# Kernel optimization log

Hardware: AMD Instinct MI355X
Metric: run time of the kernel (lower is better)

The kernel has to match this reference:

```python
import jax, jax.numpy as jnp
import numpy as np

QUERY_DIM = 1024
KEY_DIM = 1024
NUM_HEADS = 16
HEAD_DIM = QUERY_DIM // NUM_HEADS


def setup_inputs() -> dict:
    key = jax.random.key(0)
    ks = jax.random.split(key, 11)
    B, Sq, Sk = 2, 2048, 2048
    s = 0.02
    return {
        "q": jax.random.normal(ks[0], (B, Sq, QUERY_DIM), jnp.float32),
        "k": jax.random.normal(ks[1], (B, Sk, KEY_DIM), jnp.float32),
        "v": jax.random.normal(ks[2], (B, Sk, KEY_DIM), jnp.float32),
        "Wq": jax.random.normal(ks[3], (QUERY_DIM, QUERY_DIM), jnp.float32) * s,
        "bq": jnp.zeros((QUERY_DIM,), jnp.float32),
        "Wk": jax.random.normal(ks[4], (KEY_DIM, QUERY_DIM), jnp.float32) * s,
        "bk": jnp.zeros((QUERY_DIM,), jnp.float32),
        "Wv": jax.random.normal(ks[5], (KEY_DIM, QUERY_DIM), jnp.float32) * s,
        "bv": jnp.zeros((QUERY_DIM,), jnp.float32),
        "Wo": jax.random.normal(ks[6], (QUERY_DIM, QUERY_DIM), jnp.float32) * s,
        "bo": jnp.zeros((QUERY_DIM,), jnp.float32),
    }


def reference(q, k, v, Wq, bq, Wk, bk, Wv, bv, Wo, bo):
    B, Sq, _ = q.shape
    Sk = k.shape[1]
    scale = HEAD_DIM ** -0.5
    # projections -> [B, H, S, Dh]
    qh = (q @ Wq + bq).reshape(B, Sq, NUM_HEADS, HEAD_DIM).transpose(0, 2, 1, 3)
    kh = (k @ Wk + bk).reshape(B, Sk, NUM_HEADS, HEAD_DIM).transpose(0, 2, 1, 3)
    vh = (v @ Wv + bv).reshape(B, Sk, NUM_HEADS, HEAD_DIM).transpose(0, 2, 1, 3)
    scores = jnp.einsum("bhqd,bhkd->bhqk", qh, kh) * scale
    attn = jax.nn.softmax(scores, axis=-1)
    out = jnp.einsum("bhqk,bhkd->bhqd", attn, vh)
    out = out.transpose(0, 2, 1, 3).reshape(B, Sq, QUERY_DIM)
    return out @ Wo + bo  # dropout is identity at inference
```

## Files before the change

### kernel.cpp

```cpp
#include <hip/hip_runtime.h>
#include <hip/hip_fp16.h>
#include <cstddef>


#define B_   2
#define S_   2048
#define D_   1024
#define H_   16
#define DH_  64

typedef _Float16 half8 __attribute__((ext_vector_type(8)));
typedef _Float16 half4 __attribute__((ext_vector_type(4)));
typedef _Float16 half2v __attribute__((ext_vector_type(2)));
typedef float floatx4 __attribute__((ext_vector_type(4)));
typedef float floatx16 __attribute__((ext_vector_type(16)));
typedef int intx4 __attribute__((ext_vector_type(4)));

#define MFMA32(a, b, c) __builtin_amdgcn_mfma_f32_16x16x32_f16((a), (b), (c), 0, 0, 0)
#define MFMA3216(a, b, c) __builtin_amdgcn_mfma_f32_32x32x16_f16((a), (b), (c), 0, 0, 0)

#if __has_builtin(__builtin_amdgcn_fdot2)
#define LP_FDOT2 1
#else
#define LP_FDOT2 0
#endif

__device__ __forceinline__ void half_swap(int& a, int& b, const int hi) {
#if __has_builtin(__builtin_amdgcn_permlane32_swap)
    (void)hi;
    auto r = __builtin_amdgcn_permlane32_swap(a, b, false, false);
    a = r[0]; b = r[1];
#else
    const int ax = __shfl_xor(a, 32, 64), bx = __shfl_xor(b, 32, 64);
    const int na = hi ? bx : a;
    b = hi ? b : ax;
    a = na;
#endif
}

__global__ __launch_bounds__(256) void prep(
    const float* __restrict__ q, const float* __restrict__ k,
    const float* __restrict__ v,
    __half* __restrict__ qf, __half* __restrict__ kf, __half* __restrict__ vf,
    const float* __restrict__ Wq, const float* __restrict__ Wk,
    const float* __restrict__ Wv, const float* __restrict__ Wo,
    __half* __restrict__ Wtq, __half* __restrict__ Wtk,
    __half* __restrict__ Wtv, __half* __restrict__ Wto)
{
    __shared__ __align__(16) __half T[64][72];
    const int tid = threadIdx.x;
    const int z = blockIdx.z;
    if (z < 3) {
        const float* srcs[3] = {q, k, v};
        __half* dsts[3] = {qf, kf, vf};
        const int i = blockIdx.x * 256 + tid;
        const float4* s = (const float4*)srcs[z];
        const float4 a = s[2 * i], b = s[2 * i + 1];
        half8 h;
        h[0] = (_Float16)a.x; h[1] = (_Float16)a.y; h[2] = (_Float16)a.z; h[3] = (_Float16)a.w;
        h[4] = (_Float16)b.x; h[5] = (_Float16)b.y; h[6] = (_Float16)b.z; h[7] = (_Float16)b.w;
        *(half8*)&dsts[z][(size_t)i * 8] = h;
        return;
    }
    if (blockIdx.x >= 256) return;
    const float* Ws[4] = {Wq, Wk, Wv, Wo};
    __half* Wts[4] = {Wtq, Wtk, Wtv, Wto};
    const int n0 = (blockIdx.x & 15) * 64, k0 = (blockIdx.x >> 4) * 64;
    for (int w = 0; w < 4; ++w) {
        const float* W = Ws[w];
        __half* Wt = Wts[w];
        #pragma unroll
        for (int p = 0; p < 4; ++p) {
            const int c = tid + p * 256;
            const int kr = c >> 4, nc = (c & 15) * 4;
            const float4 a = *(const float4*)&W[(size_t)(k0 + kr) * D_ + n0 + nc];
            T[nc + 0][kr] = __float2half(a.x);
            T[nc + 1][kr] = __float2half(a.y);
            T[nc + 2][kr] = __float2half(a.z);
            T[nc + 3][kr] = __float2half(a.w);
        }
        __syncthreads();
        #pragma unroll
        for (int p = 0; p < 2; ++p) {
            const int c = tid + p * 256;
            const int nr = c >> 3, kc = (c & 7) * 8;
            *(half8*)&Wt[(size_t)(n0 + nr) * D_ + k0 + kc] = *(const half8*)&T[nr][kc];
        }
        __syncthreads();
    }
}

__device__ __forceinline__ void gemm_core(
    const __half* __restrict__ A, const __half* __restrict__ Bt,
    const float* __restrict__ bias, void* __restrict__ dst,
    const int mode, const float oscale)
{
    __shared__ __align__(16) char gsm[36864];
    __half (*As)[72] = (__half(*)[72])gsm;
    __half (*Bs)[72] = (__half(*)[72])(gsm + 18432);

    const int tid = threadIdx.x;
    const int m0 = blockIdx.y * 128, n0 = blockIdx.x * 128;
    const int lane = tid & 63, wv = tid >> 6;
    const int quad = lane >> 4, lr = lane & 15;
    const int wm0 = (wv >> 1) * 64, wn0 = (wv & 1) * 64;

    floatx4 acc[4][4];
    #pragma unroll
    for (int i = 0; i < 4; ++i)
        #pragma unroll
        for (int j = 0; j < 4; ++j)
            acc[i][j] = (floatx4){0.f, 0.f, 0.f, 0.f};

    half8 pa[4], pb[4];
    #pragma unroll
    for (int p = 0; p < 4; ++p) {
        const int c = tid + p * 256;
        const int row = c >> 3, seg = (c & 7) * 8;
        pa[p] = *(const half8*)&A [(size_t)(m0 + row) * D_ + seg];
        pb[p] = *(const half8*)&Bt[(size_t)(n0 + row) * D_ + seg];
    }

    for (int k0 = 0; k0 < D_; k0 += 64) {
        __syncthreads();
        #pragma unroll
        for (int p = 0; p < 4; ++p) {
            const int c = tid + p * 256;
            const int row = c >> 3, seg = (c & 7) * 8;
            *(half8*)&As[row][seg] = pa[p];
            *(half8*)&Bs[row][seg] = pb[p];
        }
        if (k0 + 64 < D_) {
            #pragma unroll
            for (int p = 0; p < 4; ++p) {
                const int c = tid + p * 256;
                const int row = c >> 3, seg = (c & 7) * 8;
                pa[p] = *(const half8*)&A [(size_t)(m0 + row) * D_ + k0 + 64 + seg];
                pb[p] = *(const half8*)&Bt[(size_t)(n0 + row) * D_ + k0 + 64 + seg];
            }
        }
        __syncthreads();
        #pragma unroll
        for (int ks = 0; ks < 2; ++ks) {
            const int ko = quad * 8 + ks * 32;
            half8 af[4], bf[4];
            #pragma unroll
            for (int i = 0; i < 4; ++i) af[i] = *(const half8*)&As[wm0 + i * 16 + lr][ko];
            #pragma unroll
            for (int j = 0; j < 4; ++j) bf[j] = *(const half8*)&Bs[wn0 + j * 16 + lr][ko];
            #pragma unroll
            for (int i = 0; i < 4; ++i)
                #pragma unroll
                for (int j = 0; j < 4; ++j)
                    acc[i][j] = MFMA32(af[i], bf[j], acc[i][j]);
        }
    }

    if (mode == 1) {
        float* out = (float*)dst;
        #pragma unroll
        for (int i = 0; i < 4; ++i) {
            #pragma unroll
            for (int j = 0; j < 4; ++j) {
                const int col = n0 + wn0 + j * 16 + lr;
                const float bval = bias[col];
                #pragma unroll
                for (int r = 0; r < 4; ++r) {
                    const int m = m0 + wm0 + i * 16 + quad * 4 + r;
                    out[(size_t)m * D_ + col] = acc[i][j][r] + bval;
                }
            }
        }
        return;
    }

    __syncthreads();
    __half (*Ct)[136] = (__half(*)[136])gsm;
    #pragma unroll
    for (int i = 0; i < 4; ++i) {
        #pragma unroll
        for (int j = 0; j < 4; ++j) {
            const int nl = wn0 + j * 16 + lr;
            const float bval = bias[n0 + nl];
            #pragma unroll
            for (int r = 0; r < 4; ++r) {
                const int ml = wm0 + i * 16 + quad * 4 + r;
                const _Float16 hv = (_Float16)((acc[i][j][r] + bval) * oscale);
                if (mode == 0) Ct[ml][nl] = hv;
                else           Ct[nl][ml] = hv;
            }
        }
    }
    __syncthreads();
    __half* oh = (__half*)dst;
    #pragma unroll
    for (int p = 0; p < 8; ++p) {
        const int row = (tid >> 4) + p * 16;
        const int cs  = (tid & 15) * 8;
        const half8 vls = *(const half8*)&Ct[row][cs];
        if (mode == 0) {
            const int m = m0 + row, col = n0 + cs;
            const int b = m >> 11, s = m & (S_ - 1);
            const int h = col >> 6, d = col & 63;
            *(half8*)&oh[(((size_t)(b * H_ + h) * S_ + s) << 6) + d] = vls;
        } else {
            const int col = n0 + row, m = m0 + cs;
            const int b = m >> 11, s = m & (S_ - 1);
            const int h = col >> 6, d = col & 63;
            *(half8*)&oh[((size_t)(b * H_ + h) * DH_ + d) * S_ + s] = vls;
        }
    }
}

__global__ __launch_bounds__(256) void gemm_proj(
    const __half* __restrict__ qf, const __half* __restrict__ kf,
    const __half* __restrict__ vf,
    const __half* __restrict__ Wtq, const __half* __restrict__ Wtk,
    const __half* __restrict__ Wtv,
    const float* __restrict__ bq, const float* __restrict__ bk,
    const float* __restrict__ bv,
    __half* __restrict__ qhf, __half* __restrict__ khf, __half* __restrict__ vht)
{
    const __half* As[3] = {qf, kf, vf};
    const __half* Bts[3] = {Wtq, Wtk, Wtv};
    const float* bs[3] = {bq, bk, bv};
    __half* ds[3] = {qhf, khf, vht};
    const int z = blockIdx.z;
    gemm_core(As[z], Bts[z], bs[z], ds[z], z == 2 ? 2 : 0,
              z == 0 ? 0.1803368801111244f : 1.0f);
}

__global__ __launch_bounds__(256) void gemm_final(
    const __half* __restrict__ attf, const __half* __restrict__ Wto,
    const float* __restrict__ bo, float* __restrict__ out)
{
    gemm_core(attf, Wto, bo, out, 1, 1.0f);
}

__global__ __launch_bounds__(512, 4) void attn_f16(
    const __half* __restrict__ qhf, const __half* __restrict__ khf,
    const __half* __restrict__ vht, __half* __restrict__ attf)
{
    __shared__ __align__(16) char smem[36864];

    const int tid = threadIdx.x;
    const int lane = tid & 63, wv = tid >> 6;
    const int l31 = lane & 31, hi = lane >> 5;
    const int kb = wv >> 2, qb = wv & 3;
    const int bh = blockIdx.y;
    const int q0 = blockIdx.x * 128;
    const size_t hbase = (size_t)bh * S_ * DH_;

    half8 qB[4];
    #pragma unroll
    for (int ds = 0; ds < 4; ++ds)
        qB[ds] = *(const half8*)&qhf[hbase
            + (size_t)(q0 + qb * 32 + l31) * DH_ + ds * 16 + hi * 8];

    float lp0 = 0.f, lp1 = 0.f;
#if !LP_FDOT2
    float lp2 = 0.f, lp3 = 0.f;
#endif
    floatx16 O[2];
    #pragma unroll
    for (int i = 0; i < 16; ++i) { O[0][i] = 0.f; O[1][i] = 0.f; }

    const int srow = tid >> 3, sseg = (tid & 7) * 8;
    const __half* kg = khf + hbase + (size_t)srow * DH_ + sseg;
    const __half* vg = vht + hbase + (size_t)srow * S_ + sseg;

    {
        __half (*K0)[72] = (__half(*)[72])smem;
        __half (*V0)[72] = (__half(*)[72])(smem + 9216);
        *(half8*)&K0[srow][sseg] = *(const half8*)kg;
        *(half8*)&V0[srow][sseg] = *(const half8*)vg;
    }
    kg += 64 * DH_; vg += 64;
    half8 pk = *(const half8*)kg;
    half8 pv = *(const half8*)vg;
    __syncthreads();

    const half2v one2 = {(_Float16)1.0f, (_Float16)1.0f};

    for (int kt = 0; kt < S_; kt += 64) {
        const int cb = (kt >> 6) & 1;
        __half (*Ks)[72] = (__half(*)[72])(smem + cb * 18432);
        __half (*Vs)[72] = (__half(*)[72])(smem + cb * 18432 + 9216);
        __half (*Kn)[72] = (__half(*)[72])(smem + (cb ^ 1) * 18432);
        __half (*Vn)[72] = (__half(*)[72])(smem + (cb ^ 1) * 18432 + 9216);

        if (kt + 64 < S_) {
            *(half8*)&Kn[srow][sseg] = pk;
            *(half8*)&Vn[srow][sseg] = pv;
            if (kt + 128 < S_) {
                kg += 64 * DH_; vg += 64;
                pk = *(const half8*)kg;
                pv = *(const half8*)vg;
            }
        }

        floatx16 s;
        #pragma unroll
        for (int i = 0; i < 16; ++i) s[i] = 0.f;
        __builtin_amdgcn_s_setprio(1);
        #pragma unroll
        for (int ds = 0; ds < 4; ++ds) {
            const half8 aK = *(const half8*)&Ks[kb * 32 + l31][ds * 16 + hi * 8];
            s = MFMA3216(aK, qB[ds], s);
        }
        __builtin_amdgcn_s_setprio(0);

        #pragma unroll
        for (int r = 0; r < 16; ++r) {
            const float e = __builtin_amdgcn_exp2f(s[r]);
#if !LP_FDOT2
            (r & 2) ? ((r & 1) ? (lp3 += e) : (lp2 += e))
                    : ((r & 1) ? (lp1 += e) : (lp0 += e));
#endif
            s[r] = e;
        }

        half8 pB[2];
        int PW[2][4];
        #pragma unroll
        for (int ks = 0; ks < 2; ++ks) {
            int P0 = __builtin_bit_cast(int, __builtin_amdgcn_cvt_pkrtz(s[ks * 8 + 0], s[ks * 8 + 1]));
            int P1 = __builtin_bit_cast(int, __builtin_amdgcn_cvt_pkrtz(s[ks * 8 + 2], s[ks * 8 + 3]));
            int P2 = __builtin_bit_cast(int, __builtin_amdgcn_cvt_pkrtz(s[ks * 8 + 4], s[ks * 8 + 5]));
            int P3 = __builtin_bit_cast(int, __builtin_amdgcn_cvt_pkrtz(s[ks * 8 + 6], s[ks * 8 + 7]));
            half_swap(P0, P2, hi);
            half_swap(P1, P3, hi);
            PW[ks][0] = P0; PW[ks][1] = P1; PW[ks][2] = P2; PW[ks][3] = P3;
            const intx4 w = {P0, P1, P2, P3};
            pB[ks] = __builtin_bit_cast(half8, w);
        }

        __builtin_amdgcn_s_setprio(1);
        #pragma unroll
        for (int db = 0; db < 2; ++db)
            #pragma unroll
            for (int ks = 0; ks < 2; ++ks) {
                const half8 aV = *(const half8*)&Vs[db * 32 + l31][kb * 32 + ks * 16 + hi * 8];
                O[db] = MFMA3216(aV, pB[ks], O[db]);
            }
        __builtin_amdgcn_s_setprio(0);

#if LP_FDOT2
        #pragma unroll
        for (int ks = 0; ks < 2; ++ks) {
            lp0 = __builtin_amdgcn_fdot2(__builtin_bit_cast(half2v, PW[ks][0]), one2, lp0, false);
            lp1 = __builtin_amdgcn_fdot2(__builtin_bit_cast(half2v, PW[ks][1]), one2, lp1, false);
            lp0 = __builtin_amdgcn_fdot2(__builtin_bit_cast(half2v, PW[ks][2]), one2, lp0, false);
            lp1 = __builtin_amdgcn_fdot2(__builtin_bit_cast(half2v, PW[ks][3]), one2, lp1, false);
        }
#endif

        __syncthreads();
    }

    float (*R)[132] = (float(*)[132])smem;
    float* Lred = (float*)(smem + 33792);

#if LP_FDOT2
    float lp = lp0 + lp1;
#else
    float lp = (lp0 + lp1) + (lp2 + lp3);
#endif
    lp += __shfl_xor(lp, 32, 64);
    const int qg = qb * 32 + l31;
    if (lane < 32) Lred[kb * 128 + qg] = lp;
    if (kb == 1) {
        #pragma unroll
        for (int db = 0; db < 2; ++db)
            #pragma unroll
            for (int r = 0; r < 16; ++r) {
                const int d = db * 32 + (r & 3) + 8 * (r >> 2) + 4 * hi;
                R[d][qg] = O[db][r];
            }
    }
    __syncthreads();
    if (kb == 0) {
        const float il = 1.0f / (Lred[qg] + Lred[128 + qg]);
        #pragma unroll
        for (int db = 0; db < 2; ++db)
            #pragma unroll
            for (int r = 0; r < 16; ++r) {
                const int d = db * 32 + (r & 3) + 8 * (r >> 2) + 4 * hi;
                O[db][r] = (O[db][r] + R[d][qg]) * il;
            }
    }
    __syncthreads();
    __half (*F)[72] = (__half(*)[72])smem;
    if (kb == 0) {
        #pragma unroll
        for (int db = 0; db < 2; ++db)
            #pragma unroll
            for (int t = 0; t < 4; ++t) {
                half4 hv;
                #pragma unroll
                for (int r = 0; r < 4; ++r) hv[r] = (_Float16)O[db][t * 4 + r];
                *(half4*)&F[qg][db * 32 + t * 8 + hi * 4] = hv;
            }
    }
    __syncthreads();

    const int b = bh >> 4, h = bh & 15;
    const int qrow = tid >> 2, dseg = (tid & 3) * 16;
    __half* dstp = &attf[(((size_t)(b * S_ + q0 + qrow)) << 10) + h * DH_ + dseg];
    *(half8*)&dstp[0] = *(const half8*)&F[qrow][dseg];
    *(half8*)&dstp[8] = *(const half8*)&F[qrow][dseg + 8];
}

extern "C" void kernel_launch(void* const* d_in, const int* in_sizes, int n_in,
                              void* d_out, int out_size, void* d_ws, size_t ws_size,
                              hipStream_t stream) {
    const float* q  = (const float*)d_in[0];
    const float* k  = (const float*)d_in[1];
    const float* v  = (const float*)d_in[2];
    const float* Wq = (const float*)d_in[3];
    const float* bq = (const float*)d_in[4];
    const float* Wk = (const float*)d_in[5];
    const float* bk = (const float*)d_in[6];
    const float* Wv = (const float*)d_in[7];
    const float* bv = (const float*)d_in[8];
    const float* Wo = (const float*)d_in[9];
    const float* bo = (const float*)d_in[10];
    float* out = (float*)d_out;

    __half* ws = (__half*)d_ws;
    const size_t NE = (size_t)B_ * S_ * D_;
    __half* qf   = ws;
    __half* kf   = ws + NE;
    __half* vf   = ws + 2 * NE;
    __half* qhf  = ws + 3 * NE;
    __half* khf  = ws + 4 * NE;
    __half* vht  = ws + 5 * NE;
    __half* attf = ws + 6 * NE;
    __half* Wtq  = ws + 7 * NE;
    __half* Wtk  = Wtq + (size_t)D_ * D_;
    __half* Wtv  = Wtk + (size_t)D_ * D_;
    __half* Wto  = Wtv + (size_t)D_ * D_;

    const dim3 blk(256);
    prep<<<dim3((unsigned)(NE / 8 / 256), 1, 4), blk, 0, stream>>>(
        q, k, v, qf, kf, vf, Wq, Wk, Wv, Wo, Wtq, Wtk, Wtv, Wto);

    gemm_proj<<<dim3(D_ / 128, (B_ * S_) / 128, 3), blk, 0, stream>>>(
        qf, kf, vf, Wtq, Wtk, Wtv, bq, bk, bv, qhf, khf, vht);

    attn_f16<<<dim3(S_ / 128, B_ * H_), dim3(512), 0, stream>>>(qhf, khf, vht, attf);

    gemm_final<<<dim3(D_ / 128, (B_ * S_) / 128), blk, 0, stream>>>(attf, Wto, bo, out);
}
```

Before: 225.1 us.

## Double-buffer GEMM LDS tiles and remap block indices for XCD locality

New measurement: 222.7 us. Within noise of the previous version (-1.0%).

```diff
diff --git a/kernel.cpp b/kernel.cpp
--- a/kernel.cpp
+++ b/kernel.cpp
@@ -93,14 +93,11 @@
 __device__ __forceinline__ void gemm_core(
     const __half* __restrict__ A, const __half* __restrict__ Bt,
     const float* __restrict__ bias, void* __restrict__ dst,
-    const int mode, const float oscale)
+    const int mode, const float oscale, const int m0, const int n0)
 {
-    __shared__ __align__(16) char gsm[36864];
-    __half (*As)[72] = (__half(*)[72])gsm;
-    __half (*Bs)[72] = (__half(*)[72])(gsm + 18432);
+    extern __shared__ __align__(16) char gsm[];
 
     const int tid = threadIdx.x;
-    const int m0 = blockIdx.y * 128, n0 = blockIdx.x * 128;
     const int lane = tid & 63, wv = tid >> 6;
     const int quad = lane >> 4, lr = lane & 15;
     const int wm0 = (wv >> 1) * 64, wn0 = (wv & 1) * 64;
@@ -111,6 +108,8 @@
         #pragma unroll
         for (int j = 0; j < 4; ++j)
             acc[i][j] = (floatx4){0.f, 0.f, 0.f, 0.f};
+
+    const int srow = tid >> 3, sseg = (tid & 7) * 8;
 
     half8 pa[4], pb[4];
     #pragma unroll
@@ -120,26 +119,53 @@
         pa[p] = *(const half8*)&A [(size_t)(m0 + row) * D_ + seg];
         pb[p] = *(const half8*)&Bt[(size_t)(n0 + row) * D_ + seg];
     }
-
-    for (int k0 = 0; k0 < D_; k0 += 64) {
-        __syncthreads();
+    {
+        __half (*As0)[72] = (__half(*)[72])gsm;
+        __half (*Bs0)[72] = (__half(*)[72])(gsm + 18432);
         #pragma unroll
         for (int p = 0; p < 4; ++p) {
             const int c = tid + p * 256;
             const int row = c >> 3, seg = (c & 7) * 8;
-            *(half8*)&As[row][seg] = pa[p];
-            *(half8*)&Bs[row][seg] = pb[p];
-        }
+            *(half8*)&As0[row][seg] = pa[p];
+            *(half8*)&Bs0[row][seg] = pb[p];
+        }
+    }
+    #pragma unroll
+    for (int p = 0; p < 4; ++p) {
+        const int c = tid + p * 256;
+        const int row = c >> 3, seg = (c & 7) * 8;
+        pa[p] = *(const half8*)&A [(size_t)(m0 + row) * D_ + 64 + seg];
+        pb[p] = *(const half8*)&Bt[(size_t)(n0 + row) * D_ + 64 + seg];
+    }
+    __syncthreads();
+
+    for (int k0 = 0; k0 < D_; k0 += 64) {
+        const int cb = (k0 >> 6) & 1;
+        __half (*As)[72] = (__half(*)[72])(gsm + cb * 36864);
+        __half (*Bs)[72] = (__half(*)[72])(gsm + cb * 36864 + 18432);
+        __half (*An)[72] = (__half(*)[72])(gsm + (cb ^ 1) * 36864);
+        __half (*Bn)[72] = (__half(*)[72])(gsm + (cb ^ 1) * 36864 + 18432);
+
         if (k0 + 64 < D_) {
             #pragma unroll
             for (int p = 0; p < 4; ++p) {
                 const int c = tid + p * 256;
                 const int row = c >> 3, seg = (c & 7) * 8;
-                pa[p] = *(const half8*)&A [(size_t)(m0 + row) * D_ + k0 + 64 + seg];
-                pb[p] = *(const half8*)&Bt[(size_t)(n0 + row) * D_ + k0 + 64 + seg];
-            }
-        }
-        __syncthreads();
+                *(half8*)&An[row][seg] = pa[p];
+                *(half8*)&Bn[row][seg] = pb[p];
+            }
+            if (k0 + 128 < D_) {
+                #pragma unroll
+                for (int p = 0; p < 4; ++p) {
+                    const int c = tid + p * 256;
+                    const int row = c >> 3, seg = (c & 7) * 8;
+                    pa[p] = *(const half8*)&A [(size_t)(m0 + row) * D_ + k0 + 128 + seg];
+                    pb[p] = *(const half8*)&Bt[(size_t)(n0 + row) * D_ + k0 + 128 + seg];
+                }
+            }
+        }
+
+        __builtin_amdgcn_s_setprio(1);
         #pragma unroll
         for (int ks = 0; ks < 2; ++ks) {
             const int ko = quad * 8 + ks * 32;
@@ -154,6 +180,9 @@
                 for (int j = 0; j < 4; ++j)
                     acc[i][j] = MFMA32(af[i], bf[j], acc[i][j]);
         }
+        __builtin_amdgcn_s_setprio(0);
+
+        __syncthreads();
     }
 
     if (mode == 1) {
@@ -174,7 +203,6 @@
         return;
     }
 
-    __syncthreads();
     __half (*Ct)[136] = (__half(*)[136])gsm;
     #pragma unroll
     for (int i = 0; i < 4; ++i) {
@@ -221,20 +249,28 @@
     const float* __restrict__ bv,
     __half* __restrict__ qhf, __half* __restrict__ khf, __half* __restrict__ vht)
 {
+    const int flat = blockIdx.x + (blockIdx.y << 3) + (blockIdx.z << 8);
+    const int wid = (flat & 7) * 96 + (flat >> 3);
+    const int z = wid >> 8;
+    const int rem = wid & 255;
+    const int m0 = (rem >> 3) * 128, n0 = (rem & 7) * 128;
+
     const __half* As[3] = {qf, kf, vf};
     const __half* Bts[3] = {Wtq, Wtk, Wtv};
     const float* bs[3] = {bq, bk, bv};
     __half* ds[3] = {qhf, khf, vht};
-    const int z = blockIdx.z;
     gemm_core(As[z], Bts[z], bs[z], ds[z], z == 2 ? 2 : 0,
-              z == 0 ? 0.1803368801111244f : 1.0f);
+              z == 0 ? 0.1803368801111244f : 1.0f, m0, n0);
 }
 
 __global__ __launch_bounds__(256) void gemm_final(
     const __half* __restrict__ attf, const __half* __restrict__ Wto,
     const float* __restrict__ bo, float* __restrict__ out)
 {
-    gemm_core(attf, Wto, bo, out, 1, 1.0f);
+    const int flat = blockIdx.x + (blockIdx.y << 3);
+    const int wid = (flat & 7) * 32 + (flat >> 3);
+    const int m0 = (wid >> 3) * 128, n0 = (wid & 7) * 128;
+    gemm_core(attf, Wto, bo, out, 1, 1.0f, m0, n0);
 }
 
 __global__ __launch_bounds__(512, 4) void attn_f16(
@@ -247,8 +283,10 @@
     const int lane = tid & 63, wv = tid >> 6;
     const int l31 = lane & 31, hi = lane >> 5;
     const int kb = wv >> 2, qb = wv & 3;
-    const int bh = blockIdx.y;
-    const int q0 = blockIdx.x * 128;
+    const int flat = blockIdx.x + (blockIdx.y << 4);
+    const int wid = ((flat & 7) << 6) + (flat >> 3);
+    const int bh = wid >> 4;
+    const int q0 = (wid & 15) * 128;
     const size_t hbase = (size_t)bh * S_ * DH_;
 
     half8 qB[4];
@@ -445,10 +483,10 @@
     prep<<<dim3((unsigned)(NE / 8 / 256), 1, 4), blk, 0, stream>>>(
         q, k, v, qf, kf, vf, Wq, Wk, Wv, Wo, Wtq, Wtk, Wtv, Wto);
 
-    gemm_proj<<<dim3(D_ / 128, (B_ * S_) / 128, 3), blk, 0, stream>>>(
+    gemm_proj<<<dim3(D_ / 128, (B_ * S_) / 128, 3), blk, 73728, stream>>>(
         qf, kf, vf, Wtq, Wtk, Wtv, bq, bk, bv, qhf, khf, vht);
 
     attn_f16<<<dim3(S_ / 128, B_ * H_), dim3(512), 0, stream>>>(qhf, khf, vht, attf);
 
-    gemm_final<<<dim3(D_ / 128, (B_ * S_) / 128), blk, 0, stream>>>(attf, Wto, bo, out);
-}
+    gemm_final<<<dim3(D_ / 128, (B_ * S_) / 128), blk, 73728, stream>>>(attf, Wto, bo, out);
+}
```

## Use direct global-to-LDS loads in GEMM and remap block IDs per XCD

Applied to the files above, without the earlier changes.

After: 222.4 us. Within noise of the previous version (-1.2%).

```diff
diff --git a/kernel.cpp b/kernel.cpp
--- a/kernel.cpp
+++ b/kernel.cpp
@@ -24,6 +24,9 @@
 #else
 #define LP_FDOT2 0
 #endif
+
+#define GLD_AS(p) ((const __attribute__((address_space(1))) void*)(p))
+#define LDS_AS(p) ((__attribute__((address_space(3))) void*)(p))
 
 __device__ __forceinline__ void half_swap(int& a, int& b, const int hi) {
 #if __has_builtin(__builtin_amdgcn_permlane32_swap)
@@ -93,14 +96,13 @@
 __device__ __forceinline__ void gemm_core(
     const __half* __restrict__ A, const __half* __restrict__ Bt,
     const float* __restrict__ bias, void* __restrict__ dst,
-    const int mode, const float oscale)
+    const int mode, const float oscale, const int m0, const int n0)
 {
-    __shared__ __align__(16) char gsm[36864];
-    __half (*As)[72] = (__half(*)[72])gsm;
-    __half (*Bs)[72] = (__half(*)[72])(gsm + 18432);
+    __shared__ __align__(16) char gsm[34816];
+    __half* Asl = (__half*)gsm;
+    __half* Bsl = (__half*)(gsm + 16384);
 
     const int tid = threadIdx.x;
-    const int m0 = blockIdx.y * 128, n0 = blockIdx.x * 128;
     const int lane = tid & 63, wv = tid >> 6;
     const int quad = lane >> 4, lr = lane & 15;
     const int wm0 = (wv >> 1) * 64, wn0 = (wv & 1) * 64;
@@ -112,48 +114,43 @@
         for (int j = 0; j < 4; ++j)
             acc[i][j] = (floatx4){0.f, 0.f, 0.f, 0.f};
 
-    half8 pa[4], pb[4];
-    #pragma unroll
-    for (int p = 0; p < 4; ++p) {
-        const int c = tid + p * 256;
-        const int row = c >> 3, seg = (c & 7) * 8;
-        pa[p] = *(const half8*)&A [(size_t)(m0 + row) * D_ + seg];
-        pb[p] = *(const half8*)&Bt[(size_t)(n0 + row) * D_ + seg];
-    }
+    const int rowb = wv * 32 + (lane >> 3);
+    const int colb = (lane & 7) * 8;
+    const __half* gA = A  + (size_t)(m0 + rowb) * D_ + colb;
+    const __half* gB = Bt + (size_t)(n0 + rowb) * D_ + colb;
 
     for (int k0 = 0; k0 < D_; k0 += 64) {
         __syncthreads();
         #pragma unroll
         for (int p = 0; p < 4; ++p) {
-            const int c = tid + p * 256;
-            const int row = c >> 3, seg = (c & 7) * 8;
-            *(half8*)&As[row][seg] = pa[p];
-            *(half8*)&Bs[row][seg] = pb[p];
-        }
-        if (k0 + 64 < D_) {
-            #pragma unroll
-            for (int p = 0; p < 4; ++p) {
-                const int c = tid + p * 256;
-                const int row = c >> 3, seg = (c & 7) * 8;
-                pa[p] = *(const half8*)&A [(size_t)(m0 + row) * D_ + k0 + 64 + seg];
-                pb[p] = *(const half8*)&Bt[(size_t)(n0 + row) * D_ + k0 + 64 + seg];
-            }
-        }
+            __builtin_amdgcn_global_load_lds(
+                GLD_AS(gA + (size_t)p * 8 * D_),
+                LDS_AS(gsm + (wv * 4 + p) * 1024), 16, 0, 0);
+            __builtin_amdgcn_global_load_lds(
+                GLD_AS(gB + (size_t)p * 8 * D_),
+                LDS_AS(gsm + 16384 + (wv * 4 + p) * 1024), 16, 0, 0);
+        }
+        gA += 64; gB += 64;
         __syncthreads();
+
+        __builtin_amdgcn_s_setprio(1);
         #pragma unroll
         for (int ks = 0; ks < 2; ++ks) {
             const int ko = quad * 8 + ks * 32;
             half8 af[4], bf[4];
             #pragma unroll
-            for (int i = 0; i < 4; ++i) af[i] = *(const half8*)&As[wm0 + i * 16 + lr][ko];
-            #pragma unroll
-            for (int j = 0; j < 4; ++j) bf[j] = *(const half8*)&Bs[wn0 + j * 16 + lr][ko];
+            for (int i = 0; i < 4; ++i)
+                af[i] = *(const half8*)&Asl[(wm0 + i * 16 + lr) * 64 + ko];
+            #pragma unroll
+            for (int j = 0; j < 4; ++j)
+                bf[j] = *(const half8*)&Bsl[(wn0 + j * 16 + lr) * 64 + ko];
             #pragma unroll
             for (int i = 0; i < 4; ++i)
                 #pragma unroll
                 for (int j = 0; j < 4; ++j)
                     acc[i][j] = MFMA32(af[i], bf[j], acc[i][j]);
         }
+        __builtin_amdgcn_s_setprio(0);
     }
 
     if (mode == 1) {
@@ -221,20 +218,28 @@
     const float* __restrict__ bv,
     __half* __restrict__ qhf, __half* __restrict__ khf, __half* __restrict__ vht)
 {
+    const int flat = blockIdx.x + (blockIdx.y << 3) + (blockIdx.z << 8);
+    const int wid = (flat & 7) * 96 + (flat >> 3);
+    const int z = wid >> 8;
+    const int rem = wid & 255;
+    const int m0 = (rem >> 3) * 128, n0 = (rem & 7) * 128;
+
     const __half* As[3] = {qf, kf, vf};
     const __half* Bts[3] = {Wtq, Wtk, Wtv};
     const float* bs[3] = {bq, bk, bv};
     __half* ds[3] = {qhf, khf, vht};
-    const int z = blockIdx.z;
     gemm_core(As[z], Bts[z], bs[z], ds[z], z == 2 ? 2 : 0,
-              z == 0 ? 0.1803368801111244f : 1.0f);
+              z == 0 ? 0.1803368801111244f : 1.0f, m0, n0);
 }
 
 __global__ __launch_bounds__(256) void gemm_final(
     const __half* __restrict__ attf, const __half* __restrict__ Wto,
     const float* __restrict__ bo, float* __restrict__ out)
 {
-    gemm_core(attf, Wto, bo, out, 1, 1.0f);
+    const int flat = blockIdx.x + (blockIdx.y << 3);
+    const int wid = (flat & 7) * 32 + (flat >> 3);
+    const int m0 = (wid >> 3) * 128, n0 = (wid & 7) * 128;
+    gemm_core(attf, Wto, bo, out, 1, 1.0f, m0, n0);
 }
 
 __global__ __launch_bounds__(512, 4) void attn_f16(
@@ -247,8 +252,10 @@
     const int lane = tid & 63, wv = tid >> 6;
     const int l31 = lane & 31, hi = lane >> 5;
     const int kb = wv >> 2, qb = wv & 3;
-    const int bh = blockIdx.y;
-    const int q0 = blockIdx.x * 128;
+    const int flat = blockIdx.x + (blockIdx.y << 4);
+    const int wid = ((flat & 7) << 6) + (flat >> 3);
+    const int bh = wid >> 4;
+    const int q0 = (wid & 15) * 128;
     const size_t hbase = (size_t)bh * S_ * DH_;
 
     half8 qB[4];
```
